# Optimization experiments

Measured on AMD Instinct MI355X. Metric: run time of the kernel, lower is better.

Reference implementation:

```python
import jax, jax.numpy as jnp
import numpy as np

# MANO prior contact vertex indices (f1+f2+f3+f4+f5+f0 from CMap_loss3)
_F1 = [697,698,699,700,712,713,714,715,737,738,739,740,741,743,744,745,746,748,749,750,753,754,755,756,757,758,759,760,761,762,763,764,765,766,767,768]
_F2 = [46,47,48,49,164,165,166,167,194,195,223,237,238,280,281,298,301,317,320,323,324,325,326,327,328,329,330,331,332,333,340,341,342,343,344,345,346,347,348,349,350,351,352,353,354,355]
_F3 = [356,357,358,359,375,376,386,387,396,397,402,403,413,429,433,434,435,436,437,438,439,440,441,442,443,444,452,453,454,455,456,459,460,461,462,463,464,465,466,467]
_F4 = [468,469,470,471,484,485,486,496,497,506,507,513,514,524,545,546,547,548,549,550,551,552,553,555,563,564,565,566,567,570,572,573,574,575,576,577,578]
_F5 = [580,581,582,583,600,601,602,614,615,624,625,630,631,641,663,664,665,666,667,668,670,672,680,681,682,683,684,686,687,688,689,690,691,692,693,694,695]
_F0 = [73,96,98,99,772,774,775,777]
PRIOR_IDX = np.array(_F1 + _F2 + _F3 + _F4 + _F5 + _F0, dtype=np.int32)


def _sqdist(a, b):
    # a: [B,N,3], b: [B,M,3] -> squared distances [B,N,M] via ||a||^2+||b||^2-2ab
    a2 = jnp.sum(a * a, -1)          # [B,N]
    b2 = jnp.sum(b * b, -1)          # [B,M]
    ab = jnp.einsum('bnd,bmd->bnm', a, b)
    return jnp.maximum(a2[:, :, None] + b2[:, None, :] - 2.0 * ab, 0.0)


def _knn1(src, trg):
    # nearest neighbor (K=1): squared dists + indices, like pytorch3d knn_points
    d2 = _sqdist(src, trg)           # [B,N,M]
    return jnp.min(d2, -1), jnp.argmin(d2, -1)


def _verts_normals(verts, faces):
    # area-weighted vertex normals (pytorch3d verts_normals_packed)
    v0 = verts[:, faces[:, 0]]       # [B,F,3]
    v1 = verts[:, faces[:, 1]]
    v2 = verts[:, faces[:, 2]]
    fn = jnp.cross(v1 - v0, v2 - v0)
    vn = jnp.zeros_like(verts)
    vn = vn.at[:, faces[:, 0]].add(fn).at[:, faces[:, 1]].add(fn).at[:, faces[:, 2]].add(fn)
    return vn / (jnp.linalg.norm(vn, axis=-1, keepdims=True) + 1e-12)


def setup_inputs() -> dict:
    key = jax.random.key(0)
    ks = jax.random.split(key, 8)
    B, N1, V, F, Z, P = 64, 8192, 778, 1538, 64, 61
    scale = 0.1  # keep points in a 0.1 box so contact thresholds (0.005/0.01) fire
    return {
        'obj_xyz': jax.random.uniform(ks[0], (B, N1, 3), jnp.float32) * scale,
        'recon_xyz': jax.random.uniform(ks[1], (B, V, 3), jnp.float32) * scale,
        'gt_xyz': jax.random.uniform(ks[2], (B, V, 3), jnp.float32) * scale,
        'mean': jax.random.normal(ks[3], (B, Z), jnp.float32),
        'log_var': jax.random.normal(ks[4], (B, Z), jnp.float32),
        'recon_param': jax.random.normal(ks[5], (B, P), jnp.float32),
        'x_param': jax.random.normal(ks[6], (B, P), jnp.float32),
        'faces': jax.random.randint(ks[7], (F, 3), 0, V, jnp.int32),
    }


def reference(obj_xyz, recon_xyz, gt_xyz, mean, log_var, recon_param, x_param, faces):
    B = obj_xyz.shape[0]
    fB = jnp.float32(B)

    # KNN from object points to gt / reconstructed hand (squared dists)
    d_gt, _ = _knn1(obj_xyz, gt_xyz)            # [B,N1]
    d_rec, idx_rec = _knn1(obj_xyz, recon_xyz)  # [B,N1], [B,N1]

    # param loss: MSE sum / B
    param_loss = jnp.sum((recon_param - x_param) ** 2) / fB

    # CVAE loss: chamfer (point_reduction='sum', batch_reduction='mean') + KLD
    d2 = _sqdist(recon_xyz, gt_xyz)             # [B,778,778]
    recon_loss = jnp.mean(jnp.sum(jnp.min(d2, -1), -1)) + jnp.mean(jnp.sum(jnp.min(d2, -2), -1))
    KLD = -0.5 * jnp.sum(1.0 + log_var - mean ** 2 - jnp.exp(log_var)) / fB * 10.0
    cvae_loss = recon_loss + KLD

    # CMap_loss3: obj NN distance to prior hand contact verts, masked by cmap
    cmap = d_rec < 0.01 ** 2                    # [B,N1] bool
    prior = recon_xyz[:, PRIOR_IDX, :]          # [B,222,3]
    obj_CD, _ = _knn1(obj_xyz, prior)           # [B,N1]
    n_points = jnp.sum(cmap).astype(jnp.float32)
    cmap_loss = 3000.0 * jnp.sum(jnp.where(cmap, obj_CD, 0.0)) / (fB * n_points)

    # CMap consistency: contact-map overlap ratio
    recon_cmap = jnp.sqrt(d_rec) < 0.005
    gt_cmap = jnp.sqrt(d_gt) < 0.005
    gt_cnum = jnp.sum(gt_cmap).astype(jnp.float32) + 0.0001
    consistency_loss = -5.0 * jnp.sum(recon_cmap & gt_cmap).astype(jnp.float32) / gt_cnum

    # inter-penetration: gather NN hand verts/normals, sign of dot, masked dist sum
    vn = _verts_normals(recon_xyz, faces)                               # [B,778,3]
    nn_v = jnp.take_along_axis(recon_xyz, idx_rec[..., None], axis=1)   # [B,N1,3]
    nn_n = jnp.take_along_axis(vn, idx_rec[..., None], axis=1)          # [B,N1,3]
    interior = jnp.sum((nn_v - obj_xyz) * nn_n, -1) > 0                 # [B,N1]
    penetr_loss = 100.0 * jnp.sum(jnp.where(interior, d_rec, 0.0)) / fB

    a, b, c, d, e = 1.0, 0.1, 1000.0, 10.0, 10.0
    loss = a * cvae_loss + b * param_loss + c * cmap_loss + d * consistency_loss + e * penetr_loss
    return loss
```

## Files before the change

### kernel.cpp

```cpp
#include <hip/hip_runtime.h>
#include <math.h>

#define NB     64
#define N1V    8192
#define NPTS   (NB * N1V)
#define NV     778
#define NVP    780
#define NQ     195
#define SEG1Q  51
#define NFACE  1538
#define NZ     64
#define NPAR   61
#define NPRIOR 204
#define PPT    8
#define BIAS   0.0625f

#define REC_BLOCKS 256
#define GT_BLOCKS  256
#define CH_BLOCKS  128
#define NROLE_BLOCKS (REC_BLOCKS + GT_BLOCKS + CH_BLOCKS)
#define CMB_BLOCKS 64

#define BATCH_F4 2352
#define ACC_OFF (NB * BATCH_F4 * 4)
#define RC_OFF  (ACC_OFF + 16)
#define GC_OFF  (RC_OFF + NPTS / 32)

__device__ __constant__ int c_prior[NPRIOR] = {
  697,698,699,700,712,713,714,715,737,738,739,740,741,743,744,745,746,748,749,750,
  753,754,755,756,757,758,759,760,761,762,763,764,765,766,767,768,
  46,47,48,49,164,165,166,167,194,195,223,237,238,280,281,298,301,317,320,323,
  324,325,326,327,328,329,330,331,332,333,340,341,342,343,344,345,346,347,348,349,
  350,351,352,353,354,355,
  356,357,358,359,375,376,386,387,396,397,402,403,413,429,433,434,435,436,437,438,
  439,440,441,442,443,444,452,453,454,455,456,459,460,461,462,463,464,465,466,467,
  468,469,470,471,484,485,486,496,497,506,507,513,514,524,545,546,547,548,549,550,
  551,552,553,555,563,564,565,566,567,570,572,573,574,575,576,577,578,
  580,581,582,583,600,601,602,614,615,624,625,630,631,641,663,664,665,666,667,668,
  670,672,680,681,682,683,684,686,687,688,689,690,691,692,693,694,695,
  73,96,98,99,772,774,775,777
};

__global__ __launch_bounds__(256) void k_prep(const float* __restrict__ recon,
                                              const float* __restrict__ gt,
                                              const int* __restrict__ faces,
                                              float4* __restrict__ ws4,
                                              float* __restrict__ acc) {
    int b = blockIdx.x, tid = threadIdx.x;
    if (b == 0 && tid < 16) acc[tid] = 0.0f;
    __shared__ float4 s_r[NV];
    __shared__ float s_vnx[NV], s_vny[NV], s_vnz[NV];
    __shared__ unsigned int s_bm[25];
    __shared__ unsigned short s_pre[26];
    __shared__ unsigned short s_perm[NV];

    if (tid < 25) s_bm[tid] = 0u;
    __syncthreads();
    if (tid < NPRIOR) {
        int v = c_prior[tid];
        atomicOr(&s_bm[v >> 5], 1u << (v & 31));
    }
    const float* rb = recon + (size_t)b * NV * 3;
    const float* gb = gt    + (size_t)b * NV * 3;
    float4* gt4   = ws4 + (size_t)b * BATCH_F4;
    float4* rec4p = gt4 + NVP;
    float4* nrm4p = rec4p + NVP;
    for (int j = tid; j < NV; j += 256) {
        float x = rb[3*j], y = rb[3*j+1], z = rb[3*j+2];
        s_r[j] = make_float4(x, y, z, x*x + y*y + z*z + BIAS);
        x = gb[3*j]; y = gb[3*j+1]; z = gb[3*j+2];
        gt4[j] = make_float4(x, y, z, x*x + y*y + z*z);
        s_vnx[j] = 0.0f; s_vny[j] = 0.0f; s_vnz[j] = 0.0f;
    }
    if (tid < 2) gt4[NV + tid] = make_float4(0.f, 0.f, 0.f, 1e30f);
    __syncthreads();
    if (tid == 0) {
        unsigned int run = 0;
        for (int w = 0; w < 25; ++w) { s_pre[w] = (unsigned short)run; run += __popc(s_bm[w]); }
        s_pre[25] = (unsigned short)run;
    }
    __syncthreads();
    for (int j = tid; j < NV; j += 256) {
        int w = j >> 5;
        unsigned int below = s_bm[w] & ((1u << (j & 31)) - 1u);
        int rank = s_pre[w] + __popc(below);
        bool member = (s_bm[w] >> (j & 31)) & 1u;
        int pos = member ? rank : (NPRIOR + (j - rank));
        s_perm[pos] = (unsigned short)j;
    }
    for (int f = tid; f < NFACE; f += 256) {
        int i0 = faces[3*f], i1 = faces[3*f+1], i2 = faces[3*f+2];
        float4 p0 = s_r[i0], p1 = s_r[i1], p2 = s_r[i2];
        float e1x = p1.x - p0.x, e1y = p1.y - p0.y, e1z = p1.z - p0.z;
        float e2x = p2.x - p0.x, e2y = p2.y - p0.y, e2z = p2.z - p0.z;
        float fx = e1y * e2z - e1z * e2y;
        float fy = e1z * e2x - e1x * e2z;
        float fz = e1x * e2y - e1y * e2x;
        atomicAdd(&s_vnx[i0], fx); atomicAdd(&s_vny[i0], fy); atomicAdd(&s_vnz[i0], fz);
        atomicAdd(&s_vnx[i1], fx); atomicAdd(&s_vny[i1], fy); atomicAdd(&s_vnz[i1], fz);
        atomicAdd(&s_vnx[i2], fx); atomicAdd(&s_vny[i2], fy); atomicAdd(&s_vnz[i2], fz);
    }
    __syncthreads();
    for (int j = tid; j < NVP; j += 256) {
        if (j < NV) {
            int src = s_perm[j];
            rec4p[j] = s_r[src];
            float x = s_vnx[src], y = s_vny[src], z = s_vnz[src];
            float inv = 1.0f / (sqrtf(x*x + y*y + z*z) + 1e-12f);
            nrm4p[j] = make_float4(x * inv, y * inv, z * inv, 0.0f);
        } else {
            rec4p[j] = make_float4(0.f, 0.f, 0.f, 1e30f);
            nrm4p[j] = make_float4(0.f, 0.f, 1.f, 0.0f);
        }
    }
}

#define LOAD_PTS(ob)                                                          \
    const float4* ob4 = (const float4*)((ob) + (size_t)tid * 24);             \
    float4 q0 = ob4[0], q1 = ob4[1], q2 = ob4[2],                             \
           q3 = ob4[3], q4 = ob4[4], q5 = ob4[5];                             \
    float px[PPT], py[PPT], pz[PPT];                                          \
    px[0]=q0.x; py[0]=q0.y; pz[0]=q0.z;  px[1]=q0.w; py[1]=q1.x; pz[1]=q1.y;  \
    px[2]=q1.z; py[2]=q1.w; pz[2]=q2.x;  px[3]=q2.y; py[3]=q2.z; pz[3]=q2.w;  \
    px[4]=q3.x; py[4]=q3.y; pz[4]=q3.z;  px[5]=q3.w; py[5]=q4.x; pz[5]=q4.y;  \
    px[6]=q4.z; py[6]=q4.w; pz[6]=q5.x;  px[7]=q5.y; py[7]=q5.z; pz[7]=q5.w;

__global__ __launch_bounds__(256) void k_fused(const float* __restrict__ obj,
                                               const float4* __restrict__ ws4,
                                               float* __restrict__ acc,
                                               unsigned char* __restrict__ rcA,
                                               unsigned char* __restrict__ gcA) {
    __shared__ float4 s_t[NVP];
    __shared__ float s_red[3];
    int tid = threadIdx.x;
    int blk = blockIdx.x;

    if (blk < REC_BLOCKS) {
        int b = blk >> 2, chunk = blk & 3;
        const float4* base = ws4 + (size_t)b * BATCH_F4;
        const float4* rec4p = base + NVP;
        const float4* nrm4p = base + 2 * NVP;
        for (int j = tid; j < NVP; j += 256) s_t[j] = rec4p[j];
        if (tid < 3) s_red[tid] = 0.0f;
        __syncthreads();

        const float* ob = obj + ((size_t)b * N1V + (size_t)chunk * 2048) * 3;
        LOAD_PTS(ob)
        float nax[PPT], nay[PPT], naz[PPT], m[PPT];
        int q[PPT];
#pragma unroll
        for (int i = 0; i < PPT; ++i) {
            nax[i] = -2.0f * px[i]; nay[i] = -2.0f * py[i]; naz[i] = -2.0f * pz[i];
            m[i] = 3.4e38f; q[i] = 0;
        }
        float mp[PPT];
#pragma unroll 1
        for (int jq = 0; jq < SEG1Q; ++jq) {
            int j = 4 * jq;
            float4 t0 = s_t[j], t1 = s_t[j+1], t2 = s_t[j+2], t3 = s_t[j+3];
#pragma unroll
            for (int i = 0; i < PPT; ++i) {
                float d0 = fmaf(nax[i], t0.x, fmaf(nay[i], t0.y, fmaf(naz[i], t0.z, t0.w)));
                float d1 = fmaf(nax[i], t1.x, fmaf(nay[i], t1.y, fmaf(naz[i], t1.z, t1.w)));
                float d2 = fmaf(nax[i], t2.x, fmaf(nay[i], t2.y, fmaf(naz[i], t2.z, t2.w)));
                float d3 = fmaf(nax[i], t3.x, fmaf(nay[i], t3.y, fmaf(naz[i], t3.z, t3.w)));
                float mn = fminf(fminf(fminf(d0, d1), fminf(d2, d3)), m[i]);
                q[i] = (mn < m[i]) ? jq : q[i];
                m[i] = mn;
            }
        }
#pragma unroll
        for (int i = 0; i < PPT; ++i) mp[i] = m[i];
#pragma unroll 1
        for (int jq = SEG1Q; jq < NQ; ++jq) {
            int j = 4 * jq;
            float4 t0 = s_t[j], t1 = s_t[j+1], t2 = s_t[j+2], t3 = s_t[j+3];
#pragma unroll
            for (int i = 0; i < PPT; ++i) {
                float d0 = fmaf(nax[i], t0.x, fmaf(nay[i], t0.y, fmaf(naz[i], t0.z, t0.w)));
                float d1 = fmaf(nax[i], t1.x, fmaf(nay[i], t1.y, fmaf(naz[i], t1.z, t1.w)));
                float d2 = fmaf(nax[i], t2.x, fmaf(nay[i], t2.y, fmaf(naz[i], t2.z, t2.w)));
                float d3 = fmaf(nax[i], t3.x, fmaf(nay[i], t3.y, fmaf(naz[i], t3.z, t3.w)));
                float mn = fminf(fminf(fminf(d0, d1), fminf(d2, d3)), m[i]);
                q[i] = (mn < m[i]) ? jq : q[i];
                m[i] = mn;
            }
        }
        float lS_cmap = 0.0f, lN_cmap = 0.0f, lS_pen = 0.0f;
        unsigned int rcbits = 0;
#pragma unroll
        for (int i = 0; i < PPT; ++i) {
            float a2 = px[i]*px[i] + py[i]*py[i] + pz[i]*pz[i];
            float drec = fmaxf(a2 + (m[i]  - BIAS), 0.0f);
            float dpri = fmaxf(a2 + (mp[i] - BIAS), 0.0f);
            bool cm = drec < 1e-4f;
            bool rc = sqrtf(drec) < 0.005f;
            if (cm) { lS_cmap += dpri; lN_cmap += 1.0f; }
            if (rc) rcbits |= (1u << i);
            int jr = 4 * q[i];
            float4 t0 = s_t[jr], t1 = s_t[jr+1], t2 = s_t[jr+2], t3 = s_t[jr+3];
            float d0 = fmaf(nax[i], t0.x, fmaf(nay[i], t0.y, fmaf(naz[i], t0.z, t0.w)));
            float d1 = fmaf(nax[i], t1.x, fmaf(nay[i], t1.y, fmaf(naz[i], t1.z, t1.w)));
            float d2 = fmaf(nax[i], t2.x, fmaf(nay[i], t2.y, fmaf(naz[i], t2.z, t2.w)));
            float d3 = fmaf(nax[i], t3.x, fmaf(nay[i], t3.y, fmaf(naz[i], t3.z, t3.w)));
            float mmin = fminf(fminf(d0, d1), fminf(d2, d3));
            int off = (d0 == mmin) ? 0 : ((d1 == mmin) ? 1 : ((d2 == mmin) ? 2 : 3));
            int jstar = jr + off;
            float4 tS = s_t[jstar];
            float4 nr = nrm4p[jstar];
            float ddot = (tS.x - px[i]) * nr.x + (tS.y - py[i]) * nr.y
                       + (tS.z - pz[i]) * nr.z;
            if (ddot > 0.0f) lS_pen += drec;
        }
        rcA[(size_t)blk * 256 + tid] = (unsigned char)rcbits;
        atomicAdd(&s_red[0], lS_cmap);
        atomicAdd(&s_red[1], lN_cmap);
        atomicAdd(&s_red[2], lS_pen);
        __syncthreads();
        if (tid == 0) atomicAdd(&acc[3], s_red[0]);
        if (tid == 1) atomicAdd(&acc[4], s_red[1]);
        if (tid == 2) atomicAdd(&acc[7], s_red[2]);
        return;
    }

    if (blk < REC_BLOCKS + GT_BLOCKS) {
        int r = blk - REC_BLOCKS;
        int b = r >> 2, chunk = r & 3;
        const float4* gt4v = ws4 + (size_t)b * BATCH_F4;
        for (int j = tid; j < NVP; j += 256) s_t[j] = gt4v[j];
        if (tid == 0) s_red[0] = 0.0f;
        __syncthreads();

        const float* ob = obj + ((size_t)b * N1V + (size_t)chunk * 2048) * 3;
        LOAD_PTS(ob)
        float nax[PPT], nay[PPT], naz[PPT], mgt[PPT];
#pragma unroll
        for (int i = 0; i < PPT; ++i) {
            nax[i] = -2.0f * px[i]; nay[i] = -2.0f * py[i]; naz[i] = -2.0f * pz[i];
            mgt[i] = 3.4e38f;
        }
#pragma unroll 1
        for (int jq = 0; jq < NQ; ++jq) {
            int j = 4 * jq;
            float4 t0 = s_t[j], t1 = s_t[j+1], t2 = s_t[j+2], t3 = s_t[j+3];
#pragma unroll
            for (int i = 0; i < PPT; ++i) {
                float d0 = fmaf(nax[i], t0.x, fmaf(nay[i], t0.y, fmaf(naz[i], t0.z, t0.w)));
                float d1 = fmaf(nax[i], t1.x, fmaf(nay[i], t1.y, fmaf(naz[i], t1.z, t1.w)));
                float d2 = fmaf(nax[i], t2.x, fmaf(nay[i], t2.y, fmaf(naz[i], t2.z, t2.w)));
                float d3 = fmaf(nax[i], t3.x, fmaf(nay[i], t3.y, fmaf(naz[i], t3.z, t3.w)));
                mgt[i] = fminf(fminf(mgt[i], fminf(d0, d1)), fminf(d2, d3));
            }
        }
        float lN_gt = 0.0f;
        unsigned int gcbits = 0;
#pragma unroll
        for (int i = 0; i < PPT; ++i) {
            float a2 = px[i]*px[i] + py[i]*py[i] + pz[i]*pz[i];
            float dgt = fmaxf(a2 + mgt[i], 0.0f);
            if (sqrtf(dgt) < 0.005f) { lN_gt += 1.0f; gcbits |= (1u << i); }
        }
        gcA[(size_t)r * 256 + tid] = (unsigned char)gcbits;
        atomicAdd(&s_red[0], lN_gt);
        __syncthreads();
        if (tid == 0) atomicAdd(&acc[5], s_red[0]);
        return;
    }

    {
        int c   = blk - (REC_BLOCKS + GT_BLOCKS);
        int b   = c >> 1;
        int dir = c & 1;
        const float4* base = ws4 + (size_t)b * BATCH_F4;
        const float4* srcv = dir ? base : (base + NVP);
        const float4* tgtv = dir ? (base + NVP) : base;
        for (int j = tid; j < NVP; j += 256) s_t[j] = tgtv[j];
        if (tid == 0) s_red[0] = 0.0f;
        __syncthreads();

        const int CPT = 4;
        float nax[CPT], nay[CPT], naz[CPT], a2[CPT], m[CPT];
        bool valid[CPT];
#pragma unroll
        for (int k = 0; k < CPT; ++k) {
            int p = tid + 256 * k;
            valid[k] = (p < NV);
            float4 s = srcv[valid[k] ? p : 0];
            nax[k] = -2.0f * s.x; nay[k] = -2.0f * s.y; naz[k] = -2.0f * s.z;
            a2[k] = s.w;
            m[k] = 3.4e38f;
        }
#pragma unroll 1
        for (int j = 0; j < NVP; j += 4) {
            float4 t0 = s_t[j], t1 = s_t[j+1], t2 = s_t[j+2], t3 = s_t[j+3];
#pragma unroll
            for (int k = 0; k < CPT; ++k) {
                float d0 = fmaf(nax[k], t0.x, fmaf(nay[k], t0.y, fmaf(naz[k], t0.z, t0.w)));
                float d1 = fmaf(nax[k], t1.x, fmaf(nay[k], t1.y, fmaf(naz[k], t1.z, t1.w)));
                float d2 = fmaf(nax[k], t2.x, fmaf(nay[k], t2.y, fmaf(naz[k], t2.z, t2.w)));
                float d3 = fmaf(nax[k], t3.x, fmaf(nay[k], t3.y, fmaf(naz[k], t3.z, t3.w)));
                m[k] = fminf(fminf(m[k], fminf(d0, d1)), fminf(d2, d3));
            }
        }
        float local = 0.0f;
#pragma unroll
        for (int k = 0; k < CPT; ++k)
            if (valid[k]) local += fmaxf(a2[k] + m[k] - BIAS, 0.0f);
        atomicAdd(&s_red[0], local);
        __syncthreads();
        if (tid == 0) atomicAdd(&acc[2], s_red[0]);
    }
}

__global__ __launch_bounds__(256) void k_combine(float* __restrict__ acc,
                                                 const unsigned int* __restrict__ rcW,
                                                 const unsigned int* __restrict__ gcW,
                                                 const float* __restrict__ mean,
                                                 const float* __restrict__ log_var,
                                                 const float* __restrict__ rp,
                                                 const float* __restrict__ xp,
                                                 float* __restrict__ out) {
    int blk = blockIdx.x, tid = threadIdx.x;
    __shared__ float s_red[2];
    __shared__ unsigned int s_ticket;
    if (tid < 2) s_red[tid] = 0.0f;
    __syncthreads();
    int idx = blk * 256 + tid;
    unsigned int rc = rcW[idx], gc = gcW[idx];
    float cnt = (float)__popc(rc & gc);
    atomicAdd(&s_red[0], cnt);
    __syncthreads();
    if (tid == 0) atomicAdd(&acc[6], s_red[0]);
    __threadfence();
    if (tid == 0) s_ticket = atomicAdd((unsigned int*)&acc[15], 1u);
    __syncthreads();

    if (s_ticket == CMB_BLOCKS - 1) {
        if (tid < 2) s_red[tid] = 0.0f;
        __syncthreads();
        float s_param = 0.0f, s_kld = 0.0f;
        for (int i = tid; i < NB * NPAR; i += 256) {
            float d = rp[i] - xp[i];
            s_param += d * d;
        }
        for (int i = tid; i < NB * NZ; i += 256) {
            float m = mean[i], lv = log_var[i];
            s_kld += 1.0f + lv - m * m - expf(lv);
        }
        atomicAdd(&s_red[0], s_param);
        atomicAdd(&s_red[1], s_kld);
        __syncthreads();
        if (tid == 0) {
            const float fB = 64.0f;
            float a2v = atomicAdd(&acc[2], 0.0f);
            float a3  = atomicAdd(&acc[3], 0.0f);
            float a4  = atomicAdd(&acc[4], 0.0f);
            float a5  = atomicAdd(&acc[5], 0.0f);
            float a6  = atomicAdd(&acc[6], 0.0f);
            float a7  = atomicAdd(&acc[7], 0.0f);
            float param_loss  = s_red[0] / fB;
            float KLD         = -0.5f * s_red[1] / fB * 10.0f;
            float recon_loss  = a2v / fB;
            float cmap_loss   = 3000.0f * a3 / (fB * a4);
            float consistency = -5.0f * a6 / (a5 + 0.0001f);
            float penetr      = 100.0f * a7 / fB;
            out[0] = (recon_loss + KLD) + 0.1f * param_loss + 1000.0f * cmap_loss
                   + 10.0f * consistency + 10.0f * penetr;
        }
    }
}

extern "C" void kernel_launch(void* const* d_in, const int* in_sizes, int n_in,
                              void* d_out, int out_size, void* d_ws, size_t ws_size,
                              hipStream_t stream) {
    (void)in_sizes; (void)n_in; (void)out_size; (void)ws_size;
    const float* obj     = (const float*)d_in[0];
    const float* recon   = (const float*)d_in[1];
    const float* gt      = (const float*)d_in[2];
    const float* mean    = (const float*)d_in[3];
    const float* log_var = (const float*)d_in[4];
    const float* rp      = (const float*)d_in[5];
    const float* xp      = (const float*)d_in[6];
    const int*   faces   = (const int*)d_in[7];
    float* acc  = (float*)d_ws + ACC_OFF;
    float4* ws4 = (float4*)d_ws;
    unsigned char* rcA = (unsigned char*)((float*)d_ws + RC_OFF);
    unsigned char* gcA = (unsigned char*)((float*)d_ws + GC_OFF);
    float* out  = (float*)d_out;

    k_prep   <<<NB,           256, 0, stream>>>(recon, gt, faces, ws4, acc);
    k_fused  <<<NROLE_BLOCKS, 256, 0, stream>>>(obj, ws4, acc, rcA, gcA);
    k_combine<<<CMB_BLOCKS,   256, 0, stream>>>(acc, (const unsigned int*)rcA,
                                                (const unsigned int*)gcA,
                                                mean, log_var, rp, xp, out);
}
```

Baseline: 197.9 us.

## Merge prep, scan and combine kernels into one persistent kernel with flag waits

Replaces the three kernel launches with a single kernel. Prep blocks publish per-batch flags, and scan blocks spin-wait on those flags before loading the hand vertices. The consistency popcount moves into the rec blocks, which wait on per-chunk gt flags, and the last-arriving block computes the final loss from per-batch accumulators. GT blocks are reordered ahead of rec blocks, the min reductions are rewritten as min3, and flags are reset with a memset. The aim is to remove launch gaps and the separate combine pass. The cost is a memset launch plus spin-wait deadlock risk if dependent blocks are not co-resident.

```diff
diff --git a/kernel.cpp b/kernel.cpp
--- a/kernel.cpp
+++ b/kernel.cpp
@@ -15,16 +15,21 @@
 #define PPT    8
 #define BIAS   0.0625f
 
-#define REC_BLOCKS 256
-#define GT_BLOCKS  256
-#define CH_BLOCKS  128
-#define NROLE_BLOCKS (REC_BLOCKS + GT_BLOCKS + CH_BLOCKS)
-#define CMB_BLOCKS 64
+#define PREP_BLOCKS 64
+#define GT_BLOCKS   256
+#define REC_BLOCKS  256
+#define CH_BLOCKS   128
+#define SCAN_BLOCKS (GT_BLOCKS + REC_BLOCKS + CH_BLOCKS)
+#define NBLOCKS     (PREP_BLOCKS + SCAN_BLOCKS)
+#define GT_BASE  PREP_BLOCKS
+#define REC_BASE (GT_BASE + GT_BLOCKS)
+#define CH_BASE  (REC_BASE + REC_BLOCKS)
 
 #define BATCH_F4 2352
-#define ACC_OFF (NB * BATCH_F4 * 4)
-#define RC_OFF  (ACC_OFF + 16)
-#define GC_OFF  (RC_OFF + NPTS / 32)
+#define ACCB_OFF  (NB * BATCH_F4 * 4)
+#define FLAGS_OFF (ACCB_OFF + NB * 8)
+#define NFLAGS    (NB + GT_BLOCKS + 1)
+#define GC_OFF    (FLAGS_OFF + NFLAGS + 3)
 
 __device__ __constant__ int c_prior[NPRIOR] = {
   697,698,699,700,712,713,714,715,737,738,739,740,741,743,744,745,746,748,749,750,
@@ -41,79 +46,18 @@
   73,96,98,99,772,774,775,777
 };
 
-__global__ __launch_bounds__(256) void k_prep(const float* __restrict__ recon,
-                                              const float* __restrict__ gt,
-                                              const int* __restrict__ faces,
-                                              float4* __restrict__ ws4,
-                                              float* __restrict__ acc) {
-    int b = blockIdx.x, tid = threadIdx.x;
-    if (b == 0 && tid < 16) acc[tid] = 0.0f;
-    __shared__ float4 s_r[NV];
-    __shared__ float s_vnx[NV], s_vny[NV], s_vnz[NV];
-    __shared__ unsigned int s_bm[25];
-    __shared__ unsigned short s_pre[26];
-    __shared__ unsigned short s_perm[NV];
-
-    if (tid < 25) s_bm[tid] = 0u;
-    __syncthreads();
-    if (tid < NPRIOR) {
-        int v = c_prior[tid];
-        atomicOr(&s_bm[v >> 5], 1u << (v & 31));
-    }
-    const float* rb = recon + (size_t)b * NV * 3;
-    const float* gb = gt    + (size_t)b * NV * 3;
-    float4* gt4   = ws4 + (size_t)b * BATCH_F4;
-    float4* rec4p = gt4 + NVP;
-    float4* nrm4p = rec4p + NVP;
-    for (int j = tid; j < NV; j += 256) {
-        float x = rb[3*j], y = rb[3*j+1], z = rb[3*j+2];
-        s_r[j] = make_float4(x, y, z, x*x + y*y + z*z + BIAS);
-        x = gb[3*j]; y = gb[3*j+1]; z = gb[3*j+2];
-        gt4[j] = make_float4(x, y, z, x*x + y*y + z*z);
-        s_vnx[j] = 0.0f; s_vny[j] = 0.0f; s_vnz[j] = 0.0f;
-    }
-    if (tid < 2) gt4[NV + tid] = make_float4(0.f, 0.f, 0.f, 1e30f);
-    __syncthreads();
-    if (tid == 0) {
-        unsigned int run = 0;
-        for (int w = 0; w < 25; ++w) { s_pre[w] = (unsigned short)run; run += __popc(s_bm[w]); }
-        s_pre[25] = (unsigned short)run;
-    }
-    __syncthreads();
-    for (int j = tid; j < NV; j += 256) {
-        int w = j >> 5;
-        unsigned int below = s_bm[w] & ((1u << (j & 31)) - 1u);
-        int rank = s_pre[w] + __popc(below);
-        bool member = (s_bm[w] >> (j & 31)) & 1u;
-        int pos = member ? rank : (NPRIOR + (j - rank));
-        s_perm[pos] = (unsigned short)j;
-    }
-    for (int f = tid; f < NFACE; f += 256) {
-        int i0 = faces[3*f], i1 = faces[3*f+1], i2 = faces[3*f+2];
-        float4 p0 = s_r[i0], p1 = s_r[i1], p2 = s_r[i2];
-        float e1x = p1.x - p0.x, e1y = p1.y - p0.y, e1z = p1.z - p0.z;
-        float e2x = p2.x - p0.x, e2y = p2.y - p0.y, e2z = p2.z - p0.z;
-        float fx = e1y * e2z - e1z * e2y;
-        float fy = e1z * e2x - e1x * e2z;
-        float fz = e1x * e2y - e1y * e2x;
-        atomicAdd(&s_vnx[i0], fx); atomicAdd(&s_vny[i0], fy); atomicAdd(&s_vnz[i0], fz);
-        atomicAdd(&s_vnx[i1], fx); atomicAdd(&s_vny[i1], fy); atomicAdd(&s_vnz[i1], fz);
-        atomicAdd(&s_vnx[i2], fx); atomicAdd(&s_vny[i2], fy); atomicAdd(&s_vnz[i2], fz);
-    }
-    __syncthreads();
-    for (int j = tid; j < NVP; j += 256) {
-        if (j < NV) {
-            int src = s_perm[j];
-            rec4p[j] = s_r[src];
-            float x = s_vnx[src], y = s_vny[src], z = s_vnz[src];
-            float inv = 1.0f / (sqrtf(x*x + y*y + z*z) + 1e-12f);
-            nrm4p[j] = make_float4(x * inv, y * inv, z * inv, 0.0f);
-        } else {
-            rec4p[j] = make_float4(0.f, 0.f, 0.f, 1e30f);
-            nrm4p[j] = make_float4(0.f, 0.f, 1.f, 0.0f);
-        }
-    }
-}
+struct PrepSh {
+    float4 r[NV];
+    float vnx[NV], vny[NV], vnz[NV];
+    unsigned int bm[25];
+    unsigned short pre[26];
+    unsigned short perm[NV];
+};
+struct ScanSh {
+    float4 t[NVP];
+    float red[8];
+};
+union ShU { PrepSh prep; ScanSh scan; };
 
 #define LOAD_PTS(ob)                                                          \
     const float4* ob4 = (const float4*)((ob) + (size_t)tid * 24);             \
@@ -125,25 +69,153 @@
     px[4]=q3.x; py[4]=q3.y; pz[4]=q3.z;  px[5]=q3.w; py[5]=q4.x; pz[5]=q4.y;  \
     px[6]=q4.z; py[6]=q4.w; pz[6]=q5.x;  px[7]=q5.y; py[7]=q5.z; pz[7]=q5.w;
 
-__global__ __launch_bounds__(256) void k_fused(const float* __restrict__ obj,
-                                               const float4* __restrict__ ws4,
-                                               float* __restrict__ acc,
-                                               unsigned char* __restrict__ rcA,
-                                               unsigned char* __restrict__ gcA) {
-    __shared__ float4 s_t[NVP];
-    __shared__ float s_red[3];
-    int tid = threadIdx.x;
-    int blk = blockIdx.x;
-
-    if (blk < REC_BLOCKS) {
-        int b = blk >> 2, chunk = blk & 3;
-        const float4* base = ws4 + (size_t)b * BATCH_F4;
-        const float4* rec4p = base + NVP;
-        const float4* nrm4p = base + 2 * NVP;
-        for (int j = tid; j < NVP; j += 256) s_t[j] = rec4p[j];
-        if (tid < 3) s_red[tid] = 0.0f;
-        __syncthreads();
-
+__device__ __forceinline__ float min3f(float a, float b, float c) {
+    return fminf(fminf(a, b), c);
+}
+
+__device__ __forceinline__ void spin_wait(unsigned int* f, int tid) {
+    if (tid == 0) {
+        while (__hip_atomic_load(f, __ATOMIC_ACQUIRE, __HIP_MEMORY_SCOPE_AGENT) == 0u)
+            __builtin_amdgcn_s_sleep(2);
+    }
+    __syncthreads();
+}
+
+__global__ __launch_bounds__(256, 4) void k_all(
+        const float* __restrict__ obj,   const float* __restrict__ recon,
+        const float* __restrict__ gt,    const int*   __restrict__ faces,
+        const float* __restrict__ mean,  const float* __restrict__ log_var,
+        const float* __restrict__ rp,    const float* __restrict__ xp,
+        float4* __restrict__ ws4,        float* __restrict__ accB,
+        unsigned int* __restrict__ flags, unsigned char* __restrict__ gcA,
+        float* __restrict__ out) {
+    __shared__ ShU sh;
+    __shared__ unsigned int s_tk;
+    int tid = threadIdx.x, blk = blockIdx.x;
+
+    if (blk < PREP_BLOCKS) {
+        int b = blk;
+        if (tid < 8) accB[b * 8 + tid] = 0.0f;
+        if (tid < 25) sh.prep.bm[tid] = 0u;
+        __syncthreads();
+        if (tid < NPRIOR) {
+            int v = c_prior[tid];
+            atomicOr(&sh.prep.bm[v >> 5], 1u << (v & 31));
+        }
+        const float* rb = recon + (size_t)b * NV * 3;
+        const float* gb = gt    + (size_t)b * NV * 3;
+        float4* gt4   = ws4 + (size_t)b * BATCH_F4;
+        float4* rec4p = gt4 + NVP;
+        float4* nrm4p = rec4p + NVP;
+        for (int j = tid; j < NV; j += 256) {
+            float x = rb[3*j], y = rb[3*j+1], z = rb[3*j+2];
+            sh.prep.r[j] = make_float4(x, y, z, x*x + y*y + z*z + BIAS);
+            x = gb[3*j]; y = gb[3*j+1]; z = gb[3*j+2];
+            gt4[j] = make_float4(x, y, z, x*x + y*y + z*z);
+            sh.prep.vnx[j] = 0.0f; sh.prep.vny[j] = 0.0f; sh.prep.vnz[j] = 0.0f;
+        }
+        if (tid < 2) gt4[NV + tid] = make_float4(0.f, 0.f, 0.f, 1e30f);
+        __syncthreads();
+        if (tid == 0) {
+            unsigned int run = 0;
+            for (int w = 0; w < 25; ++w) { sh.prep.pre[w] = (unsigned short)run; run += __popc(sh.prep.bm[w]); }
+            sh.prep.pre[25] = (unsigned short)run;
+        }
+        __syncthreads();
+        for (int j = tid; j < NV; j += 256) {
+            int w = j >> 5;
+            unsigned int below = sh.prep.bm[w] & ((1u << (j & 31)) - 1u);
+            int rank = sh.prep.pre[w] + __popc(below);
+            bool member = (sh.prep.bm[w] >> (j & 31)) & 1u;
+            int pos = member ? rank : (NPRIOR + (j - rank));
+            sh.prep.perm[pos] = (unsigned short)j;
+        }
+        for (int f = tid; f < NFACE; f += 256) {
+            int i0 = faces[3*f], i1 = faces[3*f+1], i2 = faces[3*f+2];
+            float4 p0 = sh.prep.r[i0], p1 = sh.prep.r[i1], p2 = sh.prep.r[i2];
+            float e1x = p1.x - p0.x, e1y = p1.y - p0.y, e1z = p1.z - p0.z;
+            float e2x = p2.x - p0.x, e2y = p2.y - p0.y, e2z = p2.z - p0.z;
+            float fx = e1y * e2z - e1z * e2y;
+            float fy = e1z * e2x - e1x * e2z;
+            float fz = e1x * e2y - e1y * e2x;
+            atomicAdd(&sh.prep.vnx[i0], fx); atomicAdd(&sh.prep.vny[i0], fy); atomicAdd(&sh.prep.vnz[i0], fz);
+            atomicAdd(&sh.prep.vnx[i1], fx); atomicAdd(&sh.prep.vny[i1], fy); atomicAdd(&sh.prep.vnz[i1], fz);
+            atomicAdd(&sh.prep.vnx[i2], fx); atomicAdd(&sh.prep.vny[i2], fy); atomicAdd(&sh.prep.vnz[i2], fz);
+        }
+        __syncthreads();
+        for (int j = tid; j < NVP; j += 256) {
+            if (j < NV) {
+                int src = sh.prep.perm[j];
+                rec4p[j] = sh.prep.r[src];
+                float x = sh.prep.vnx[src], y = sh.prep.vny[src], z = sh.prep.vnz[src];
+                float inv = 1.0f / (sqrtf(x*x + y*y + z*z) + 1e-12f);
+                nrm4p[j] = make_float4(x * inv, y * inv, z * inv, 0.0f);
+            } else {
+                rec4p[j] = make_float4(0.f, 0.f, 0.f, 1e30f);
+                nrm4p[j] = make_float4(0.f, 0.f, 1.f, 0.0f);
+            }
+        }
+        __syncthreads();
+        if (tid == 0) {
+            __threadfence();
+            __hip_atomic_store(&flags[b], 1u, __ATOMIC_RELEASE, __HIP_MEMORY_SCOPE_AGENT);
+        }
+        return;
+    }
+
+    float4* s_t = sh.scan.t;
+    float*  red = sh.scan.red;
+
+    if (blk < REC_BASE) {
+        int r = blk - GT_BASE;
+        int b = r >> 2, chunk = r & 3;
+        const float* ob = obj + ((size_t)b * N1V + (size_t)chunk * 2048) * 3;
+        LOAD_PTS(ob)
+        float nax[PPT], nay[PPT], naz[PPT], mgt[PPT];
+#pragma unroll
+        for (int i = 0; i < PPT; ++i) {
+            nax[i] = -2.0f * px[i]; nay[i] = -2.0f * py[i]; naz[i] = -2.0f * pz[i];
+            mgt[i] = 3.4e38f;
+        }
+        spin_wait(&flags[b], tid);
+        const float4* gt4v = ws4 + (size_t)b * BATCH_F4;
+        for (int j = tid; j < NVP; j += 256) s_t[j] = gt4v[j];
+        if (tid == 0) red[0] = 0.0f;
+        __syncthreads();
+
+#pragma unroll 1
+        for (int jq = 0; jq < NQ; ++jq) {
+            int j = 4 * jq;
+            float4 t0 = s_t[j], t1 = s_t[j+1], t2 = s_t[j+2], t3 = s_t[j+3];
+#pragma unroll
+            for (int i = 0; i < PPT; ++i) {
+                float d0 = fmaf(nax[i], t0.x, fmaf(nay[i], t0.y, fmaf(naz[i], t0.z, t0.w)));
+                float d1 = fmaf(nax[i], t1.x, fmaf(nay[i], t1.y, fmaf(naz[i], t1.z, t1.w)));
+                float d2 = fmaf(nax[i], t2.x, fmaf(nay[i], t2.y, fmaf(naz[i], t2.z, t2.w)));
+                float d3 = fmaf(nax[i], t3.x, fmaf(nay[i], t3.y, fmaf(naz[i], t3.z, t3.w)));
+                float u = min3f(d0, d1, d2);
+                mgt[i] = min3f(u, d3, mgt[i]);
+            }
+        }
+        float lN_gt = 0.0f;
+        unsigned int gcbits = 0;
+#pragma unroll
+        for (int i = 0; i < PPT; ++i) {
+            float a2 = px[i]*px[i] + py[i]*py[i] + pz[i]*pz[i];
+            float dgt = fmaxf(a2 + mgt[i], 0.0f);
+            if (sqrtf(dgt) < 0.005f) { lN_gt += 1.0f; gcbits |= (1u << i); }
+        }
+        gcA[(size_t)r * 256 + tid] = (unsigned char)gcbits;
+        atomicAdd(&red[0], lN_gt);
+        __syncthreads();
+        if (tid == 0) {
+            __threadfence();
+            __hip_atomic_store(&flags[NB + r], 1u, __ATOMIC_RELEASE, __HIP_MEMORY_SCOPE_AGENT);
+            atomicAdd(&accB[b * 8 + 3], red[0]);
+        }
+    } else if (blk < CH_BASE) {
+        int r = blk - REC_BASE;
+        int b = r >> 2, chunk = r & 3;
         const float* ob = obj + ((size_t)b * N1V + (size_t)chunk * 2048) * 3;
         LOAD_PTS(ob)
         float nax[PPT], nay[PPT], naz[PPT], m[PPT];
@@ -153,6 +225,14 @@
             nax[i] = -2.0f * px[i]; nay[i] = -2.0f * py[i]; naz[i] = -2.0f * pz[i];
             m[i] = 3.4e38f; q[i] = 0;
         }
+        spin_wait(&flags[b], tid);
+        const float4* base  = ws4 + (size_t)b * BATCH_F4;
+        const float4* rec4p = base + NVP;
+        const float4* nrm4p = base + 2 * NVP;
+        for (int j = tid; j < NVP; j += 256) s_t[j] = rec4p[j];
+        if (tid < 4) red[tid] = 0.0f;
+        __syncthreads();
+
         float mp[PPT];
 #pragma unroll 1
         for (int jq = 0; jq < SEG1Q; ++jq) {
@@ -164,7 +244,8 @@
                 float d1 = fmaf(nax[i], t1.x, fmaf(nay[i], t1.y, fmaf(naz[i], t1.z, t1.w)));
                 float d2 = fmaf(nax[i], t2.x, fmaf(nay[i], t2.y, fmaf(naz[i], t2.z, t2.w)));
                 float d3 = fmaf(nax[i], t3.x, fmaf(nay[i], t3.y, fmaf(naz[i], t3.z, t3.w)));
-                float mn = fminf(fminf(fminf(d0, d1), fminf(d2, d3)), m[i]);
+                float u  = min3f(d0, d1, d2);
+                float mn = min3f(u, d3, m[i]);
                 q[i] = (mn < m[i]) ? jq : q[i];
                 m[i] = mn;
             }
@@ -181,7 +262,8 @@
                 float d1 = fmaf(nax[i], t1.x, fmaf(nay[i], t1.y, fmaf(naz[i], t1.z, t1.w)));
                 float d2 = fmaf(nax[i], t2.x, fmaf(nay[i], t2.y, fmaf(naz[i], t2.z, t2.w)));
                 float d3 = fmaf(nax[i], t3.x, fmaf(nay[i], t3.y, fmaf(naz[i], t3.z, t3.w)));
-                float mn = fminf(fminf(fminf(d0, d1), fminf(d2, d3)), m[i]);
+                float u  = min3f(d0, d1, d2);
+                float mn = min3f(u, d3, m[i]);
                 q[i] = (mn < m[i]) ? jq : q[i];
                 m[i] = mn;
             }
@@ -212,70 +294,28 @@
                        + (tS.z - pz[i]) * nr.z;
             if (ddot > 0.0f) lS_pen += drec;
         }
-        rcA[(size_t)blk * 256 + tid] = (unsigned char)rcbits;
-        atomicAdd(&s_red[0], lS_cmap);
-        atomicAdd(&s_red[1], lN_cmap);
-        atomicAdd(&s_red[2], lS_pen);
-        __syncthreads();
-        if (tid == 0) atomicAdd(&acc[3], s_red[0]);
-        if (tid == 1) atomicAdd(&acc[4], s_red[1]);
-        if (tid == 2) atomicAdd(&acc[7], s_red[2]);
-        return;
-    }
-
-    if (blk < REC_BLOCKS + GT_BLOCKS) {
-        int r = blk - REC_BLOCKS;
-        int b = r >> 2, chunk = r & 3;
-        const float4* gt4v = ws4 + (size_t)b * BATCH_F4;
-        for (int j = tid; j < NVP; j += 256) s_t[j] = gt4v[j];
-        if (tid == 0) s_red[0] = 0.0f;
-        __syncthreads();
-
-        const float* ob = obj + ((size_t)b * N1V + (size_t)chunk * 2048) * 3;
-        LOAD_PTS(ob)
-        float nax[PPT], nay[PPT], naz[PPT], mgt[PPT];
-#pragma unroll
-        for (int i = 0; i < PPT; ++i) {
-            nax[i] = -2.0f * px[i]; nay[i] = -2.0f * py[i]; naz[i] = -2.0f * pz[i];
-            mgt[i] = 3.4e38f;
-        }
-#pragma unroll 1
-        for (int jq = 0; jq < NQ; ++jq) {
-            int j = 4 * jq;
-            float4 t0 = s_t[j], t1 = s_t[j+1], t2 = s_t[j+2], t3 = s_t[j+3];
-#pragma unroll
-            for (int i = 0; i < PPT; ++i) {
-                float d0 = fmaf(nax[i], t0.x, fmaf(nay[i], t0.y, fmaf(naz[i], t0.z, t0.w)));
-                float d1 = fmaf(nax[i], t1.x, fmaf(nay[i], t1.y, fmaf(naz[i], t1.z, t1.w)));
-                float d2 = fmaf(nax[i], t2.x, fmaf(nay[i], t2.y, fmaf(naz[i], t2.z, t2.w)));
-                float d3 = fmaf(nax[i], t3.x, fmaf(nay[i], t3.y, fmaf(naz[i], t3.z, t3.w)));
-                mgt[i] = fminf(fminf(mgt[i], fminf(d0, d1)), fminf(d2, d3));
-            }
-        }
-        float lN_gt = 0.0f;
-        unsigned int gcbits = 0;
-#pragma unroll
-        for (int i = 0; i < PPT; ++i) {
-            float a2 = px[i]*px[i] + py[i]*py[i] + pz[i]*pz[i];
-            float dgt = fmaxf(a2 + mgt[i], 0.0f);
-            if (sqrtf(dgt) < 0.005f) { lN_gt += 1.0f; gcbits |= (1u << i); }
-        }
-        gcA[(size_t)r * 256 + tid] = (unsigned char)gcbits;
-        atomicAdd(&s_red[0], lN_gt);
-        __syncthreads();
-        if (tid == 0) atomicAdd(&acc[5], s_red[0]);
-        return;
-    }
-
-    {
-        int c   = blk - (REC_BLOCKS + GT_BLOCKS);
+        atomicAdd(&red[0], lS_cmap);
+        atomicAdd(&red[1], lN_cmap);
+        atomicAdd(&red[2], lS_pen);
+        spin_wait(&flags[NB + r], tid);
+        unsigned int gcb = gcA[(size_t)r * 256 + tid];
+        float lcons = (float)__popc(rcbits & gcb);
+        atomicAdd(&red[3], lcons);
+        __syncthreads();
+        if (tid == 0) atomicAdd(&accB[b * 8 + 1], red[0]);
+        if (tid == 1) atomicAdd(&accB[b * 8 + 2], red[1]);
+        if (tid == 2) atomicAdd(&accB[b * 8 + 5], red[2]);
+        if (tid == 3) atomicAdd(&accB[b * 8 + 4], red[3]);
+    } else {
+        int c   = blk - CH_BASE;
         int b   = c >> 1;
         int dir = c & 1;
+        spin_wait(&flags[b], tid);
         const float4* base = ws4 + (size_t)b * BATCH_F4;
         const float4* srcv = dir ? base : (base + NVP);
         const float4* tgtv = dir ? (base + NVP) : base;
         for (int j = tid; j < NVP; j += 256) s_t[j] = tgtv[j];
-        if (tid == 0) s_red[0] = 0.0f;
+        if (tid == 0) red[0] = 0.0f;
         __syncthreads();
 
         const int CPT = 4;
@@ -299,71 +339,60 @@
                 float d1 = fmaf(nax[k], t1.x, fmaf(nay[k], t1.y, fmaf(naz[k], t1.z, t1.w)));
                 float d2 = fmaf(nax[k], t2.x, fmaf(nay[k], t2.y, fmaf(naz[k], t2.z, t2.w)));
                 float d3 = fmaf(nax[k], t3.x, fmaf(nay[k], t3.y, fmaf(naz[k], t3.z, t3.w)));
-                m[k] = fminf(fminf(m[k], fminf(d0, d1)), fminf(d2, d3));
+                float u = min3f(d0, d1, d2);
+                m[k] = min3f(u, d3, m[k]);
             }
         }
         float local = 0.0f;
 #pragma unroll
         for (int k = 0; k < CPT; ++k)
             if (valid[k]) local += fmaxf(a2[k] + m[k] - BIAS, 0.0f);
-        atomicAdd(&s_red[0], local);
-        __syncthreads();
-        if (tid == 0) atomicAdd(&acc[2], s_red[0]);
+        atomicAdd(&red[0], local);
+        __syncthreads();
+        if (tid == 0) atomicAdd(&accB[b * 8 + 0], red[0]);
     }
-}
-
-__global__ __launch_bounds__(256) void k_combine(float* __restrict__ acc,
-                                                 const unsigned int* __restrict__ rcW,
-                                                 const unsigned int* __restrict__ gcW,
-                                                 const float* __restrict__ mean,
-                                                 const float* __restrict__ log_var,
-                                                 const float* __restrict__ rp,
-                                                 const float* __restrict__ xp,
-                                                 float* __restrict__ out) {
-    int blk = blockIdx.x, tid = threadIdx.x;
-    __shared__ float s_red[2];
-    __shared__ unsigned int s_ticket;
-    if (tid < 2) s_red[tid] = 0.0f;
+
     __syncthreads();
-    int idx = blk * 256 + tid;
-    unsigned int rc = rcW[idx], gc = gcW[idx];
-    float cnt = (float)__popc(rc & gc);
-    atomicAdd(&s_red[0], cnt);
+    if (tid == 0) {
+        __threadfence();
+        s_tk = atomicAdd(&flags[NB + GT_BLOCKS], 1u);
+    }
     __syncthreads();
-    if (tid == 0) atomicAdd(&acc[6], s_red[0]);
-    __threadfence();
-    if (tid == 0) s_ticket = atomicAdd((unsigned int*)&acc[15], 1u);
-    __syncthreads();
-
-    if (s_ticket == CMB_BLOCKS - 1) {
-        if (tid < 2) s_red[tid] = 0.0f;
-        __syncthreads();
+    if (s_tk == SCAN_BLOCKS - 1) {
+        if (tid < 8) red[tid] = 0.0f;
+        __syncthreads();
+        float l0=0.f,l1=0.f,l2=0.f,l3=0.f,l4=0.f,l5=0.f;
+        for (int b2 = tid; b2 < NB; b2 += 256) {
+            const float* row = accB + (size_t)b2 * 8;
+            l0 += __hip_atomic_load(row + 0, __ATOMIC_RELAXED, __HIP_MEMORY_SCOPE_AGENT);
+            l1 += __hip_atomic_load(row + 1, __ATOMIC_RELAXED, __HIP_MEMORY_SCOPE_AGENT);
+            l2 += __hip_atomic_load(row + 2, __ATOMIC_RELAXED, __HIP_MEMORY_SCOPE_AGENT);
+            l3 += __hip_atomic_load(row + 3, __ATOMIC_RELAXED, __HIP_MEMORY_SCOPE_AGENT);
+            l4 += __hip_atomic_load(row + 4, __ATOMIC_RELAXED, __HIP_MEMORY_SCOPE_AGENT);
+            l5 += __hip_atomic_load(row + 5, __ATOMIC_RELAXED, __HIP_MEMORY_SCOPE_AGENT);
+        }
+        atomicAdd(&red[0], l0); atomicAdd(&red[1], l1); atomicAdd(&red[2], l2);
+        atomicAdd(&red[3], l3); atomicAdd(&red[4], l4); atomicAdd(&red[5], l5);
         float s_param = 0.0f, s_kld = 0.0f;
         for (int i = tid; i < NB * NPAR; i += 256) {
             float d = rp[i] - xp[i];
             s_param += d * d;
         }
         for (int i = tid; i < NB * NZ; i += 256) {
-            float m = mean[i], lv = log_var[i];
-            s_kld += 1.0f + lv - m * m - expf(lv);
-        }
-        atomicAdd(&s_red[0], s_param);
-        atomicAdd(&s_red[1], s_kld);
+            float mv = mean[i], lv = log_var[i];
+            s_kld += 1.0f + lv - mv * mv - expf(lv);
+        }
+        atomicAdd(&red[6], s_param);
+        atomicAdd(&red[7], s_kld);
         __syncthreads();
         if (tid == 0) {
             const float fB = 64.0f;
-            float a2v = atomicAdd(&acc[2], 0.0f);
-            float a3  = atomicAdd(&acc[3], 0.0f);
-            float a4  = atomicAdd(&acc[4], 0.0f);
-            float a5  = atomicAdd(&acc[5], 0.0f);
-            float a6  = atomicAdd(&acc[6], 0.0f);
-            float a7  = atomicAdd(&acc[7], 0.0f);
-            float param_loss  = s_red[0] / fB;
-            float KLD         = -0.5f * s_red[1] / fB * 10.0f;
-            float recon_loss  = a2v / fB;
-            float cmap_loss   = 3000.0f * a3 / (fB * a4);
-            float consistency = -5.0f * a6 / (a5 + 0.0001f);
-            float penetr      = 100.0f * a7 / fB;
+            float recon_loss  = red[0] / fB;
+            float cmap_loss   = 3000.0f * red[1] / (fB * red[2]);
+            float consistency = -5.0f * red[4] / (red[3] + 0.0001f);
+            float penetr      = 100.0f * red[5] / fB;
+            float param_loss  = red[6] / fB;
+            float KLD         = -0.5f * red[7] / fB * 10.0f;
             out[0] = (recon_loss + KLD) + 0.1f * param_loss + 1000.0f * cmap_loss
                    + 10.0f * consistency + 10.0f * penetr;
         }
@@ -382,15 +411,14 @@
     const float* rp      = (const float*)d_in[5];
     const float* xp      = (const float*)d_in[6];
     const int*   faces   = (const int*)d_in[7];
-    float* acc  = (float*)d_ws + ACC_OFF;
+    float* wsf = (float*)d_ws;
     float4* ws4 = (float4*)d_ws;
-    unsigned char* rcA = (unsigned char*)((float*)d_ws + RC_OFF);
-    unsigned char* gcA = (unsigned char*)((float*)d_ws + GC_OFF);
-    float* out  = (float*)d_out;
-
-    k_prep   <<<NB,           256, 0, stream>>>(recon, gt, faces, ws4, acc);
-    k_fused  <<<NROLE_BLOCKS, 256, 0, stream>>>(obj, ws4, acc, rcA, gcA);
-    k_combine<<<CMB_BLOCKS,   256, 0, stream>>>(acc, (const unsigned int*)rcA,
-                                                (const unsigned int*)gcA,
-                                                mean, log_var, rp, xp, out);
+    float* accB = wsf + ACCB_OFF;
+    unsigned int* flags = (unsigned int*)(wsf + FLAGS_OFF);
+    unsigned char* gcA = (unsigned char*)(wsf + GC_OFF);
+    float* out = (float*)d_out;
+
+    hipMemsetAsync(flags, 0, NFLAGS * sizeof(unsigned int), stream);
+    k_all<<<NBLOCKS, 256, 0, stream>>>(obj, recon, gt, faces, mean, log_var,
+                                       rp, xp, ws4, accB, flags, gcA, out);
 }
```

New measurement: 244.8 us. +23.7%, slower.
